# Kernel optimization log

Measured on AMD Instinct MI355X. Metric: run time of the kernel, lower is better.

Reference implementation:

```python
import jax, jax.numpy as jnp
import numpy as np

B, S, IN, OUT = 4, 2048, 4096, 1024
ROUNDS = 12  # prime_factors(4096) == [2]*12
QMIN, QMAX = -128, 127


def _create_noise(key, shape, lo, hi):
    # Obfuscation noise spanning the data range; exactly corrected in forward.
    return jax.random.uniform(key, shape, jnp.float32, -0.5, 0.5) * (hi - lo)


def setup_inputs() -> dict:
    key = jax.random.key(0)
    ks = jax.random.split(key, 6)
    x = jax.random.normal(ks[0], (B, S, IN), jnp.float32)
    weight = jax.random.normal(ks[1], (OUT, IN), jnp.float32) * 0.02
    bias = jax.random.normal(ks[2], (OUT,), jnp.float32) * 0.02
    weight_noise = _create_noise(ks[3], (OUT, IN), weight.min(), weight.max())
    noise_x = _create_noise(ks[4], (B, S, IN), x.min(), x.max())
    # one random permutation of in_features per round
    perms = jnp.stack([jax.random.permutation(jax.random.fold_in(key, 1000 + r), IN)
                       for r in range(ROUNDS)]).astype(jnp.int32)
    # 2048 random orthogonal 2x2 blocks per round (rotations, like ortho_group with dim=2)
    theta = jax.random.uniform(ks[5], (ROUNDS, IN // 2), jnp.float32, 0.0, 2.0 * np.pi)
    c, s = jnp.cos(theta), jnp.sin(theta)
    row0 = jnp.stack([c, -s], axis=-1)
    row1 = jnp.stack([s, c], axis=-1)
    matrices = jnp.stack([row0, row1], axis=-2)  # (ROUNDS, IN//2, 2, 2)
    return {"x": x, "weight": weight, "bias": bias, "weight_noise": weight_noise,
            "noise_x": noise_x, "permutations": perms, "matrices": matrices}


def _permute_matrix_operation(X, perms, mats):
    # X: (..., n, cols). Each round: gather rows by permutation, then apply a
    # block-diagonal orthogonal transform (G blocks of size f along the n axis).
    lead = X.shape[:-2]
    n, cols = X.shape[-2], X.shape[-1]
    G, f = mats.shape[1], mats.shape[2]
    for r in range(mats.shape[0]):
        X = jnp.take(X, perms[r], axis=-2)
        Xb = X.reshape(lead + (G, f, cols))
        X = jnp.einsum('gij,...gjc->...gic', mats[r], Xb).reshape(lead + (n, cols))
    return X


def _quant_dequant(t):
    # Asymmetric per-tensor quantize -> round -> clamp -> dequantize (int8-style).
    lo, hi = t.min(), t.max()
    scale = (hi - lo) / (QMAX - QMIN)
    zp = jnp.round(QMIN - lo / scale)
    q = jnp.clip(jnp.round(t / scale + zp), QMIN, QMAX)
    return (q - zp) * scale


def reference(x, weight, bias, weight_noise, noise_x, permutations, matrices):
    # inverse-transpose blocks; equals `matrices` for orthogonal blocks, kept explicit for fidelity
    inv_mats_mT = jnp.swapaxes(jnp.linalg.inv(matrices), -1, -2)
    w_plus = weight + weight_noise                                   # (OUT, IN)
    permuted_w = jnp.swapaxes(
        _permute_matrix_operation(jnp.swapaxes(w_plus, -1, -2), permutations, inv_mats_mT), -1, -2)
    qw = _quant_dequant(permuted_w)                                  # (OUT, IN)
    permuted_x = jnp.swapaxes(
        _permute_matrix_operation(jnp.swapaxes(x + noise_x, -1, -2), permutations, matrices), -1, -2)
    qx = _quant_dequant(permuted_x)                                  # (B, S, IN)
    res = qx @ qw.T + bias                                           # quantized matmul + bias
    res = res - x @ weight_noise.T                                   # correction term 1
    res = res - noise_x @ w_plus.T                                   # correction term 2
    return res
```

## Files before the change

### kernel.cpp

```cpp
#include <hip/hip_runtime.h>


#define IN_F   4096
#define OUT_F  1024
#define MROWS  8192
#define KTOT   12288
#define KHALF  6144
#define NPASS  6
#define NTIL   96

typedef _Float16 f16;
typedef _Float16 f16x8 __attribute__((ext_vector_type(8)));
typedef _Float16 f16x4 __attribute__((ext_vector_type(4)));
typedef float    f32x4 __attribute__((ext_vector_type(4)));

#define OFF_XT  (0ull)
#define OFF_WT  (OFF_XT + (size_t)MROWS * IN_F * 4)
#define OFF_A   (OFF_WT + (size_t)OUT_F * IN_F * 4)
#define OFF_B   (OFF_A + (size_t)MROWS * KTOT * 2)
#define OFF_MM  (OFF_B + (size_t)OUT_F * KTOT * 2)
#define OFF_TIX (OFF_MM + 256)
#define OFF_TCX (OFF_TIX + (size_t)NPASS * 2048 * 8)
#define OFF_TIW (OFF_TCX + (size_t)NPASS * 2048 * 32)
#define OFF_TCW (OFF_TIW + (size_t)NPASS * 2048 * 8)

#define SW(s) ((s) ^ (((s) >> 3) & 7))

__device__ __forceinline__ unsigned enc_f(float f) {
  unsigned u = __float_as_uint(f);
  return (u & 0x80000000u) ? ~u : (u | 0x80000000u);
}
__device__ __forceinline__ float dec_f(unsigned u) {
  unsigned b = (u & 0x80000000u) ? (u & 0x7fffffffu) : ~u;
  return __uint_as_float(b);
}

__device__ __forceinline__ float4 f4comb(float4 c, float4 x0, float4 x1,
                                         float4 x2, float4 x3) {
  return make_float4(c.x * x0.x + c.y * x1.x + c.z * x2.x + c.w * x3.x,
                     c.x * x0.y + c.y * x1.y + c.z * x2.y + c.w * x3.y,
                     c.x * x0.z + c.y * x1.z + c.z * x2.z + c.w * x3.z,
                     c.x * x0.w + c.y * x1.w + c.z * x2.w + c.w * x3.w);
}

__global__ void build_tables_kernel(const int* __restrict__ perms,
                                    const float* __restrict__ mats,
                                    uint2* __restrict__ tIx, float4* __restrict__ tCx,
                                    uint2* __restrict__ tIw, float4* __restrict__ tCw,
                                    unsigned* __restrict__ mm) {
  if (blockIdx.x == 0 && threadIdx.x == 0) {
    mm[0] = 0xFFFFFFFFu; mm[1] = 0u; mm[2] = 0xFFFFFFFFu; mm[3] = 0u;
  }
  int p = blockIdx.x;
  int r0 = 2 * p, r1 = 2 * p + 1;
  for (int g = threadIdx.x; g < 2048; g += blockDim.x) {
    int q0 = perms[r1 * IN_F + 2 * g], q1 = perms[r1 * IN_F + 2 * g + 1];
    int a0 = q0 >> 1, e0 = q0 & 1, a1 = q1 >> 1, e1 = q1 & 1;
    unsigned i0 = perms[r0 * IN_F + 2 * a0], i1 = perms[r0 * IN_F + 2 * a0 + 1];
    unsigned i2 = perms[r0 * IN_F + 2 * a1], i3 = perms[r0 * IN_F + 2 * a1 + 1];
    uint2 idx = make_uint2(i0 | (i1 << 16), i2 | (i3 << 16));
    const float* Ma = mats + ((size_t)r0 * 2048 + a0) * 4;
    const float* Mb = mats + ((size_t)r0 * 2048 + a1) * 4;
    const float* M1 = mats + ((size_t)r1 * 2048 + g) * 4;
    int o = p * 2048 + g;
    {
      float c00 = Ma[e0 * 2], c01 = Ma[e0 * 2 + 1];
      float c10 = Mb[e1 * 2], c11 = Mb[e1 * 2 + 1];
      float m00 = M1[0], m01 = M1[1], m10 = M1[2], m11 = M1[3];
      tIx[o] = idx;
      tCx[2 * o]     = make_float4(m00 * c00, m00 * c01, m01 * c10, m01 * c11);
      tCx[2 * o + 1] = make_float4(m10 * c00, m10 * c01, m11 * c10, m11 * c11);
    }
    {
      float rda = 1.0f / (Ma[0] * Ma[3] - Ma[1] * Ma[2]);
      float rdb = 1.0f / (Mb[0] * Mb[3] - Mb[1] * Mb[2]);
      float rd1 = 1.0f / (M1[0] * M1[3] - M1[1] * M1[2]);
      float c00 = (e0 == 0 ? Ma[3] : -Ma[1]) * rda;
      float c01 = (e0 == 0 ? -Ma[2] : Ma[0]) * rda;
      float c10 = (e1 == 0 ? Mb[3] : -Mb[1]) * rdb;
      float c11 = (e1 == 0 ? -Mb[2] : Mb[0]) * rdb;
      float m00 = M1[3] * rd1, m01 = -M1[2] * rd1;
      float m10 = -M1[1] * rd1, m11 = M1[0] * rd1;
      tIw[o] = idx;
      tCw[2 * o]     = make_float4(m00 * c00, m00 * c01, m01 * c10, m01 * c11);
      tCw[2 * o + 1] = make_float4(m10 * c00, m10 * c01, m11 * c10, m11 * c11);
    }
  }
}

__global__ __launch_bounds__(1024) void transform_kernel(
    const float* __restrict__ x, const float* __restrict__ nx,
    const float* __restrict__ w, const float* __restrict__ wn,
    const uint2* __restrict__ tIx, const float4* __restrict__ tCx,
    const uint2* __restrict__ tIw, const float4* __restrict__ tCw,
    float* __restrict__ xt, float* __restrict__ wt,
    f16* __restrict__ Aall, f16* __restrict__ Ball,
    unsigned* __restrict__ mm) {
  extern __shared__ float4 buf[];
  const int t = threadIdx.x;
  const bool isW = blockIdx.x >= (MROWS / 4);
  const float *in0, *in1; const uint2* tI; const float4* tC;
  float* tout; f16* fout; int mmidx; size_t m0;
  if (!isW) {
    m0 = (size_t)blockIdx.x * 4;
    in0 = x; in1 = nx; tI = tIx; tC = tCx; tout = xt; fout = Aall; mmidx = 0;
  } else {
    m0 = (size_t)(blockIdx.x - MROWS / 4) * 4;
    in0 = w; in1 = wn; tI = tIw; tC = tCw; tout = wt; fout = Ball; mmidx = 2;
  }

  {
    float4 a0 = ((const float4*)(in0 + (m0 + 0) * IN_F))[t];
    float4 a1 = ((const float4*)(in0 + (m0 + 1) * IN_F))[t];
    float4 a2 = ((const float4*)(in0 + (m0 + 2) * IN_F))[t];
    float4 a3 = ((const float4*)(in0 + (m0 + 3) * IN_F))[t];
    float4 b0 = ((const float4*)(in1 + (m0 + 0) * IN_F))[t];
    float4 b1 = ((const float4*)(in1 + (m0 + 1) * IN_F))[t];
    float4 b2 = ((const float4*)(in1 + (m0 + 2) * IN_F))[t];
    float4 b3 = ((const float4*)(in1 + (m0 + 3) * IN_F))[t];
    float4 s0 = make_float4(a0.x + b0.x, a0.y + b0.y, a0.z + b0.z, a0.w + b0.w);
    float4 s1 = make_float4(a1.x + b1.x, a1.y + b1.y, a1.z + b1.z, a1.w + b1.w);
    float4 s2 = make_float4(a2.x + b2.x, a2.y + b2.y, a2.z + b2.z, a2.w + b2.w);
    float4 s3 = make_float4(a3.x + b3.x, a3.y + b3.y, a3.z + b3.z, a3.w + b3.w);
    int c = t * 4;
    buf[SW(c + 0)] = make_float4(s0.x, s1.x, s2.x, s3.x);
    buf[SW(c + 1)] = make_float4(s0.y, s1.y, s2.y, s3.y);
    buf[SW(c + 2)] = make_float4(s0.z, s1.z, s2.z, s3.z);
    buf[SW(c + 3)] = make_float4(s0.w, s1.w, s2.w, s3.w);
#pragma unroll
    for (int r = 0; r < 4; r++) {
      float4 av = r == 0 ? a0 : r == 1 ? a1 : r == 2 ? a2 : a3;
      float4 bv = r == 0 ? b0 : r == 1 ? b1 : r == 2 ? b2 : b3;
      float4 sv = r == 0 ? s0 : r == 1 ? s1 : r == 2 ? s2 : s3;
      f16* fr = fout + (m0 + r) * KTOT;
      f16x4 p, q;
      if (isW) {
        p.x=(f16)bv.x; p.y=(f16)bv.y; p.z=(f16)bv.z; p.w=(f16)bv.w;
        q.x=(f16)sv.x; q.y=(f16)sv.y; q.z=(f16)sv.z; q.w=(f16)sv.w;
      } else {
        p.x=(f16)(-av.x); p.y=(f16)(-av.y); p.z=(f16)(-av.z); p.w=(f16)(-av.w);
        q.x=(f16)(-bv.x); q.y=(f16)(-bv.y); q.z=(f16)(-bv.z); q.w=(f16)(-bv.w);
      }
      *(f16x4*)(fr + IN_F + c)     = p;
      *(f16x4*)(fr + 2 * IN_F + c) = q;
    }
  }
  __syncthreads();

  int cur = 0;
  for (int pass = 0; pass < NPASS; pass++) {
    const uint2* ti = tI + pass * 2048;
    const float4* tc = tC + (size_t)pass * 4096;
    const float4* bc = buf + cur * 4096;
    float4* bn = buf + (cur ^ 1) * 4096;
#pragma unroll
    for (int i = 0; i < 2; i++) {
      int g = i * 1024 + t;
      uint2 pk = ti[g];
      float4 cA = tc[2 * g], cB = tc[2 * g + 1];
      float4 x0 = bc[SW(pk.x & 0xffff)], x1 = bc[SW(pk.x >> 16)];
      float4 x2 = bc[SW(pk.y & 0xffff)], x3 = bc[SW(pk.y >> 16)];
      bn[SW(2 * g)]     = f4comb(cA, x0, x1, x2, x3);
      bn[SW(2 * g + 1)] = f4comb(cB, x0, x1, x2, x3);
    }
    cur ^= 1;
    __syncthreads();
  }
  float lmin = 3.4e38f, lmax = -3.4e38f;
  {
    int c = t * 4;
    float4 q0 = buf[SW(c + 0)];
    float4 q1 = buf[SW(c + 1)];
    float4 q2 = buf[SW(c + 2)];
    float4 q3 = buf[SW(c + 3)];
    ((float4*)(tout + (m0 + 0) * IN_F))[t] = make_float4(q0.x, q1.x, q2.x, q3.x);
    ((float4*)(tout + (m0 + 1) * IN_F))[t] = make_float4(q0.y, q1.y, q2.y, q3.y);
    ((float4*)(tout + (m0 + 2) * IN_F))[t] = make_float4(q0.z, q1.z, q2.z, q3.z);
    ((float4*)(tout + (m0 + 3) * IN_F))[t] = make_float4(q0.w, q1.w, q2.w, q3.w);
    float mn0 = fminf(fminf(q0.x, q0.y), fminf(q0.z, q0.w));
    float mn1 = fminf(fminf(q1.x, q1.y), fminf(q1.z, q1.w));
    float mn2 = fminf(fminf(q2.x, q2.y), fminf(q2.z, q2.w));
    float mn3 = fminf(fminf(q3.x, q3.y), fminf(q3.z, q3.w));
    float mx0 = fmaxf(fmaxf(q0.x, q0.y), fmaxf(q0.z, q0.w));
    float mx1 = fmaxf(fmaxf(q1.x, q1.y), fmaxf(q1.z, q1.w));
    float mx2 = fmaxf(fmaxf(q2.x, q2.y), fmaxf(q2.z, q2.w));
    float mx3 = fmaxf(fmaxf(q3.x, q3.y), fmaxf(q3.z, q3.w));
    lmin = fminf(fminf(mn0, mn1), fminf(mn2, mn3));
    lmax = fmaxf(fmaxf(mx0, mx1), fmaxf(mx2, mx3));
  }
#pragma unroll
  for (int off = 32; off > 0; off >>= 1) {
    lmin = fminf(lmin, __shfl_down(lmin, off));
    lmax = fmaxf(lmax, __shfl_down(lmax, off));
  }
  float* red = (float*)(buf + 4096);
  int wid = t >> 6;
  if ((t & 63) == 0) { red[wid * 2] = lmin; red[wid * 2 + 1] = lmax; }
  __syncthreads();
  if (t == 0) {
    float bmin = red[0], bmax = red[1];
#pragma unroll
    for (int i = 1; i < 16; i++) {
      bmin = fminf(bmin, red[i * 2]);
      bmax = fmaxf(bmax, red[i * 2 + 1]);
    }
    atomicMin(&mm[mmidx], enc_f(bmin));
    atomicMax(&mm[mmidx + 1], enc_f(bmax));
  }
}

__global__ void finalize_kernel(unsigned* mm) {
  float* sc = (float*)(mm + 4);
  float xlo = dec_f(mm[0]), xhi = dec_f(mm[1]);
  float wlo = dec_f(mm[2]), whi = dec_f(mm[3]);
  float sx = (xhi - xlo) / 255.0f;
  float zx = rintf(-128.0f - xlo / sx);
  float sw = (whi - wlo) / 255.0f;
  float zw = rintf(-128.0f - wlo / sw);
  sc[0] = sx; sc[1] = zx; sc[2] = sw; sc[3] = zw;
}

__global__ __launch_bounds__(256) void quant_kernel(
    const float* __restrict__ xt, const float* __restrict__ wt,
    f16* __restrict__ Aall, f16* __restrict__ Ball,
    const unsigned* __restrict__ mm) {
  const float* sc = (const float*)(mm + 4);
  const bool isW = blockIdx.x >= (MROWS / 4);
  size_t m0 = (size_t)(isW ? blockIdx.x - MROWS / 4 : blockIdx.x) * 4;
  float s = isW ? sc[2] : sc[0], zp = isW ? sc[3] : sc[1];
  int t = threadIdx.x;
#pragma unroll
  for (int r = 0; r < 4; r++) {
    const float4* srow = (const float4*)((isW ? wt : xt) + (m0 + r) * IN_F);
    f16* drow = (isW ? Ball : Aall) + (m0 + r) * KTOT;
#pragma unroll
    for (int j = 0; j < 4; j++) {
      int i4 = j * 256 + t;
      float4 v = srow[i4];
      float q0 = (fminf(fmaxf(rintf(v.x / s + zp), -128.f), 127.f) - zp) * s;
      float q1 = (fminf(fmaxf(rintf(v.y / s + zp), -128.f), 127.f) - zp) * s;
      float q2 = (fminf(fmaxf(rintf(v.z / s + zp), -128.f), 127.f) - zp) * s;
      float q3 = (fminf(fmaxf(rintf(v.w / s + zp), -128.f), 127.f) - zp) * s;
      f16x4 o; o.x = (f16)q0; o.y = (f16)q1; o.z = (f16)q2; o.w = (f16)q3;
      *(f16x4*)(drow + i4 * 4) = o;
    }
  }
}

__global__ __launch_bounds__(256) void bias_init_kernel(
    const float* __restrict__ bias, float* __restrict__ out) {
  const float4* b4 = (const float4*)bias;
  float4* o4 = (float4*)out;
  int idx = blockIdx.x * 256 + threadIdx.x;
  const int total = MROWS * OUT_F / 4;
  for (int i = idx; i < total; i += gridDim.x * 256)
    o4[i] = b4[i & (OUT_F / 4 - 1)];
}

__device__ __forceinline__ void gl2lds16(const void* g, void* l) {
  __builtin_amdgcn_global_load_lds(
      (__attribute__((address_space(1))) void*)g,
      (__attribute__((address_space(3))) void*)l, 16, 0, 0);
}

#define GBAR() asm volatile("s_barrier" ::: "memory")
#define MFMA16(d, va, vb) d = __builtin_amdgcn_mfma_f32_16x16x32_f16(va, vb, d, 0, 0, 0)

#define STAGE(t, hh) do {                                                   \
    const int c_ = (t) & 1;                                                 \
    if ((hh) < 2) {                                                         \
      const f16* g_ = gA + (size_t)((hh) * 128) * KTOT + (size_t)(t) * 64;  \
      f16* l_ = As + c_ * 16384 + (hh) * 8192 + sbase;                      \
      gl2lds16(g_, l_);                                                     \
      gl2lds16(g_ + (size_t)64 * KTOT, l_ + 4096);                          \
    } else {                                                                \
      const f16* g_ = gB + (size_t)(((hh) - 2) * 128) * KTOT + (size_t)(t) * 64; \
      f16* l_ = Bs + c_ * 16384 + ((hh) - 2) * 8192 + sbase;                \
      gl2lds16(g_, l_);                                                     \
      gl2lds16(g_ + (size_t)64 * KTOT, l_ + 4096);                          \
    }                                                                       \
  } while (0)

__global__ __launch_bounds__(512, 2) void gemm_kernel(
    const f16* __restrict__ A, const f16* __restrict__ B,
    float* __restrict__ out) {
  extern __shared__ f16 sm[];
  f16* As = sm;
  f16* Bs = sm + 32768;

  const int tid = threadIdx.x;
  const int wave = tid >> 6, lane = tid & 63;
  const int fr = lane & 15, quad = lane >> 4;
  const int wm = wave >> 2, wn = wave & 3;

  const int orig = blockIdx.x;
  const int wg = (orig & 7) * 32 + (orig >> 3);
  const int ks = wg >> 7;
  const int rem = wg & 127;
  const int bn = rem >> 5, bm = rem & 31;
  const size_t k0 = (size_t)ks * KHALF;

  const int srow = (wave << 3) + (lane >> 3);
  const int scol = (((lane & 7) ^ (lane >> 3)) << 3);
  const f16* gA = A + ((size_t)bm * 256 + srow) * KTOT + k0 + scol;
  const f16* gB = B + ((size_t)bn * 256 + srow) * KTOT + k0 + scol;
  const int sbase = wave << 9;

  const int co0 = ((quad ^ (fr & 7)) << 3);
  const int co1 = co0 ^ 32;
  const f16* rA0 = As + wm * 8192 + fr * 64 + co0;
  const f16* rA1 = As + wm * 8192 + fr * 64 + co1;
  const f16* rB0 = Bs + (wn >> 1) * 8192 + (wn & 1) * 4096 + fr * 64 + co0;
  const f16* rB1 = Bs + (wn >> 1) * 8192 + (wn & 1) * 4096 + fr * 64 + co1;

  f16x8 a0[4][2], a1[4][2], bF[4][2];
  f32x4 acc[8][4] = {};

  STAGE(0, 0); STAGE(0, 1); STAGE(0, 2); STAGE(0, 3);
  STAGE(1, 0); STAGE(1, 1);
  asm volatile("s_waitcnt vmcnt(4)" ::: "memory");
  GBAR();

  for (int t = 0; t < NTIL; ++t) {
    const int c = t & 1;
    const f16* pa0 = rA0 + c * 16384;
    const f16* pa1 = rA1 + c * 16384;
    const f16* pb0 = rB0 + c * 16384;
    const f16* pb1 = rB1 + c * 16384;

#pragma unroll
    for (int i = 0; i < 4; i++) {
      a0[i][0] = *(const f16x8*)(pa0 + i * 1024);
      a0[i][1] = *(const f16x8*)(pa1 + i * 1024);
    }
#pragma unroll
    for (int j = 0; j < 2; j++) {
      bF[j][0] = *(const f16x8*)(pb0 + j * 1024);
      bF[j][1] = *(const f16x8*)(pb1 + j * 1024);
    }
#pragma unroll
    for (int j = 0; j < 2; j++) {
      bF[2 + j][0] = *(const f16x8*)(pb0 + (2 + j) * 1024);
      bF[2 + j][1] = *(const f16x8*)(pb1 + (2 + j) * 1024);
    }
#pragma unroll
    for (int i = 0; i < 4; i++) {
      a1[i][0] = *(const f16x8*)(pa0 + (4 + i) * 1024);
      a1[i][1] = *(const f16x8*)(pa1 + (4 + i) * 1024);
    }
    if (t + 1 < NTIL) STAGE(t + 1, 2);
    GBAR();
    __builtin_amdgcn_s_setprio(1);
#pragma unroll
    for (int i = 0; i < 4; i++)
#pragma unroll
      for (int j = 0; j < 2; j++) {
        MFMA16(acc[i][j], a0[i][0], bF[j][0]);
        MFMA16(acc[i][j], a0[i][1], bF[j][1]);
      }
    __builtin_amdgcn_s_setprio(0);
    GBAR();

    if (t + 1 < NTIL) STAGE(t + 1, 3);
    GBAR();
    __builtin_amdgcn_s_setprio(1);
#pragma unroll
    for (int i = 0; i < 4; i++)
#pragma unroll
      for (int j = 0; j < 2; j++) {
        MFMA16(acc[i][2 + j], a0[i][0], bF[2 + j][0]);
        MFMA16(acc[i][2 + j], a0[i][1], bF[2 + j][1]);
      }
    __builtin_amdgcn_s_setprio(0);
    GBAR();

    if (t + 2 < NTIL) STAGE(t + 2, 0);
    GBAR();
    __builtin_amdgcn_s_setprio(1);
#pragma unroll
    for (int i = 0; i < 4; i++)
#pragma unroll
      for (int j = 0; j < 2; j++) {
        MFMA16(acc[4 + i][j], a1[i][0], bF[j][0]);
        MFMA16(acc[4 + i][j], a1[i][1], bF[j][1]);
      }
    __builtin_amdgcn_s_setprio(0);
    GBAR();

    if (t + 2 < NTIL) STAGE(t + 2, 1);
    GBAR();
    __builtin_amdgcn_s_setprio(1);
#pragma unroll
    for (int i = 0; i < 4; i++)
#pragma unroll
      for (int j = 0; j < 2; j++) {
        MFMA16(acc[4 + i][2 + j], a1[i][0], bF[2 + j][0]);
        MFMA16(acc[4 + i][2 + j], a1[i][1], bF[2 + j][1]);
      }
    __builtin_amdgcn_s_setprio(0);
    if (t + 2 < NTIL) {
      asm volatile("s_waitcnt vmcnt(4)" ::: "memory");
    } else if (t + 1 < NTIL) {
      asm volatile("s_waitcnt vmcnt(0)" ::: "memory");
    }
    GBAR();
  }

  const size_t orow = (size_t)bm * 256 + wm * 128 + quad * 4;
  const int ocol = bn * 256 + wn * 64 + fr;
#pragma unroll
  for (int mi = 0; mi < 8; mi++)
#pragma unroll
    for (int ni = 0; ni < 4; ni++)
#pragma unroll
      for (int e = 0; e < 4; e++)
        unsafeAtomicAdd(&out[(orow + mi * 16 + e) * OUT_F + (ocol + ni * 16)],
                        acc[mi][ni][e]);
}

extern "C" void kernel_launch(void* const* d_in, const int* in_sizes, int n_in,
                              void* d_out, int out_size, void* d_ws, size_t ws_size,
                              hipStream_t stream) {
  const float* x     = (const float*)d_in[0];
  const float* w     = (const float*)d_in[1];
  const float* bias  = (const float*)d_in[2];
  const float* wn    = (const float*)d_in[3];
  const float* nx    = (const float*)d_in[4];
  const int*   perms = (const int*)d_in[5];
  const float* mats  = (const float*)d_in[6];
  float* out = (float*)d_out;

  char* ws = (char*)d_ws;
  float* xt   = (float*)(ws + OFF_XT);
  float* wt   = (float*)(ws + OFF_WT);
  f16*   Aall = (f16*)(ws + OFF_A);
  f16*   Ball = (f16*)(ws + OFF_B);
  unsigned* mm = (unsigned*)(ws + OFF_MM);
  uint2*  tIx = (uint2*)(ws + OFF_TIX);
  float4* tCx = (float4*)(ws + OFF_TCX);
  uint2*  tIw = (uint2*)(ws + OFF_TIW);
  float4* tCw = (float4*)(ws + OFF_TCW);

  static int attr_set = 0;
  if (!attr_set) {
    (void)hipFuncSetAttribute(reinterpret_cast<const void*>(gemm_kernel),
                              hipFuncAttributeMaxDynamicSharedMemorySize, 131072);
    (void)hipFuncSetAttribute(reinterpret_cast<const void*>(transform_kernel),
                              hipFuncAttributeMaxDynamicSharedMemorySize, 131072);
    attr_set = 1;
  }

  build_tables_kernel<<<NPASS, 256, 0, stream>>>(perms, mats, tIx, tCx, tIw, tCw, mm);
  transform_kernel<<<MROWS / 4 + OUT_F / 4, 1024, 131072, stream>>>(
      x, nx, w, wn, tIx, tCx, tIw, tCw, xt, wt, Aall, Ball, mm);
  finalize_kernel<<<1, 1, 0, stream>>>(mm);
  quant_kernel<<<(MROWS + OUT_F) / 4, 256, 0, stream>>>(xt, wt, Aall, Ball, mm);
  bias_init_kernel<<<1024, 256, 0, stream>>>(bias, out);
  gemm_kernel<<<2 * (MROWS / 256) * (OUT_F / 256), 512, 131072, stream>>>(Aall, Ball, out);
}
```

Measured before the change: 684.1 us.

## Merge GEMM barrier phases, fuse bias init into quant, widen table build grid

The GEMM main loop drops from four barrier-separated MFMA phases per tile to two. Each phase now issues two global-to-LDS stages, and an lgkmcnt wait is added before the middle barrier, which cuts synchronisation overhead. The bias-initialisation kernel is folded into the quant kernel as extra blocks, removing one launch. The table-building kernel now uses 48 blocks with one element per thread instead of 6 looping blocks. Fewer barriers may reduce the overlap between loads and MFMAs and change the LDS race margins.

```diff
diff --git a/kernel.cpp b/kernel.cpp
--- a/kernel.cpp
+++ b/kernel.cpp
@@ -43,17 +43,18 @@
                      c.x * x0.w + c.y * x1.w + c.z * x2.w + c.w * x3.w);
 }
 
-__global__ void build_tables_kernel(const int* __restrict__ perms,
-                                    const float* __restrict__ mats,
-                                    uint2* __restrict__ tIx, float4* __restrict__ tCx,
-                                    uint2* __restrict__ tIw, float4* __restrict__ tCw,
-                                    unsigned* __restrict__ mm) {
+__global__ __launch_bounds__(256) void build_tables_kernel(
+    const int* __restrict__ perms, const float* __restrict__ mats,
+    uint2* __restrict__ tIx, float4* __restrict__ tCx,
+    uint2* __restrict__ tIw, float4* __restrict__ tCw,
+    unsigned* __restrict__ mm) {
   if (blockIdx.x == 0 && threadIdx.x == 0) {
     mm[0] = 0xFFFFFFFFu; mm[1] = 0u; mm[2] = 0xFFFFFFFFu; mm[3] = 0u;
   }
-  int p = blockIdx.x;
+  int p = blockIdx.x >> 3;
+  int g = ((blockIdx.x & 7) << 8) + threadIdx.x;
   int r0 = 2 * p, r1 = 2 * p + 1;
-  for (int g = threadIdx.x; g < 2048; g += blockDim.x) {
+  {
     int q0 = perms[r1 * IN_F + 2 * g], q1 = perms[r1 * IN_F + 2 * g + 1];
     int a0 = q0 >> 1, e0 = q0 & 1, a1 = q1 >> 1, e1 = q1 & 1;
     unsigned i0 = perms[r0 * IN_F + 2 * a0], i1 = perms[r0 * IN_F + 2 * a0 + 1];
@@ -220,10 +221,21 @@
   sc[0] = sx; sc[1] = zx; sc[2] = sw; sc[3] = zw;
 }
 
+#define NQB ((MROWS + OUT_F) / 4)
 __global__ __launch_bounds__(256) void quant_kernel(
     const float* __restrict__ xt, const float* __restrict__ wt,
     f16* __restrict__ Aall, f16* __restrict__ Ball,
-    const unsigned* __restrict__ mm) {
+    const unsigned* __restrict__ mm,
+    const float* __restrict__ bias, float* __restrict__ out) {
+  if (blockIdx.x >= NQB) {
+    const float4* b4 = (const float4*)bias;
+    float4* o4 = (float4*)out;
+    int idx = (blockIdx.x - NQB) * 256 + threadIdx.x;
+    const int total = MROWS * OUT_F / 4;
+    for (int i = idx; i < total; i += 512 * 256)
+      o4[i] = b4[i & (OUT_F / 4 - 1)];
+    return;
+  }
   const float* sc = (const float*)(mm + 4);
   const bool isW = blockIdx.x >= (MROWS / 4);
   size_t m0 = (size_t)(isW ? blockIdx.x - MROWS / 4 : blockIdx.x) * 4;
@@ -245,16 +257,6 @@
       *(f16x4*)(drow + i4 * 4) = o;
     }
   }
-}
-
-__global__ __launch_bounds__(256) void bias_init_kernel(
-    const float* __restrict__ bias, float* __restrict__ out) {
-  const float4* b4 = (const float4*)bias;
-  float4* o4 = (float4*)out;
-  int idx = blockIdx.x * 256 + threadIdx.x;
-  const int total = MROWS * OUT_F / 4;
-  for (int i = idx; i < total; i += gridDim.x * 256)
-    o4[i] = b4[i & (OUT_F / 4 - 1)];
 }
 
 __device__ __forceinline__ void gl2lds16(const void* g, void* l) {
@@ -334,70 +336,41 @@
       a0[i][1] = *(const f16x8*)(pa1 + i * 1024);
     }
 #pragma unroll
-    for (int j = 0; j < 2; j++) {
+    for (int j = 0; j < 4; j++) {
       bF[j][0] = *(const f16x8*)(pb0 + j * 1024);
       bF[j][1] = *(const f16x8*)(pb1 + j * 1024);
-    }
-#pragma unroll
-    for (int j = 0; j < 2; j++) {
-      bF[2 + j][0] = *(const f16x8*)(pb0 + (2 + j) * 1024);
-      bF[2 + j][1] = *(const f16x8*)(pb1 + (2 + j) * 1024);
     }
 #pragma unroll
     for (int i = 0; i < 4; i++) {
       a1[i][0] = *(const f16x8*)(pa0 + (4 + i) * 1024);
       a1[i][1] = *(const f16x8*)(pa1 + (4 + i) * 1024);
     }
-    if (t + 1 < NTIL) STAGE(t + 1, 2);
-    GBAR();
+    if (t + 1 < NTIL) { STAGE(t + 1, 2); STAGE(t + 1, 3); }
+
     __builtin_amdgcn_s_setprio(1);
 #pragma unroll
     for (int i = 0; i < 4; i++)
 #pragma unroll
-      for (int j = 0; j < 2; j++) {
+      for (int j = 0; j < 4; j++) {
         MFMA16(acc[i][j], a0[i][0], bF[j][0]);
         MFMA16(acc[i][j], a0[i][1], bF[j][1]);
       }
     __builtin_amdgcn_s_setprio(0);
+
+    asm volatile("s_waitcnt lgkmcnt(0)" ::: "memory");
     GBAR();
-
-    if (t + 1 < NTIL) STAGE(t + 1, 3);
-    GBAR();
+    if (t + 2 < NTIL) { STAGE(t + 2, 0); STAGE(t + 2, 1); }
+
     __builtin_amdgcn_s_setprio(1);
 #pragma unroll
     for (int i = 0; i < 4; i++)
 #pragma unroll
-      for (int j = 0; j < 2; j++) {
-        MFMA16(acc[i][2 + j], a0[i][0], bF[2 + j][0]);
-        MFMA16(acc[i][2 + j], a0[i][1], bF[2 + j][1]);
-      }
-    __builtin_amdgcn_s_setprio(0);
-    GBAR();
-
-    if (t + 2 < NTIL) STAGE(t + 2, 0);
-    GBAR();
-    __builtin_amdgcn_s_setprio(1);
-#pragma unroll
-    for (int i = 0; i < 4; i++)
-#pragma unroll
-      for (int j = 0; j < 2; j++) {
+      for (int j = 0; j < 4; j++) {
         MFMA16(acc[4 + i][j], a1[i][0], bF[j][0]);
         MFMA16(acc[4 + i][j], a1[i][1], bF[j][1]);
       }
     __builtin_amdgcn_s_setprio(0);
-    GBAR();
-
-    if (t + 2 < NTIL) STAGE(t + 2, 1);
-    GBAR();
-    __builtin_amdgcn_s_setprio(1);
-#pragma unroll
-    for (int i = 0; i < 4; i++)
-#pragma unroll
-      for (int j = 0; j < 2; j++) {
-        MFMA16(acc[4 + i][2 + j], a1[i][0], bF[2 + j][0]);
-        MFMA16(acc[4 + i][2 + j], a1[i][1], bF[2 + j][1]);
-      }
-    __builtin_amdgcn_s_setprio(0);
+
     if (t + 2 < NTIL) {
       asm volatile("s_waitcnt vmcnt(4)" ::: "memory");
     } else if (t + 1 < NTIL) {
@@ -450,11 +423,10 @@
     attr_set = 1;
   }
 
-  build_tables_kernel<<<NPASS, 256, 0, stream>>>(perms, mats, tIx, tCx, tIw, tCw, mm);
+  build_tables_kernel<<<48, 256, 0, stream>>>(perms, mats, tIx, tCx, tIw, tCw, mm);
   transform_kernel<<<MROWS / 4 + OUT_F / 4, 1024, 131072, stream>>>(
       x, nx, w, wn, tIx, tCx, tIw, tCw, xt, wt, Aall, Ball, mm);
   finalize_kernel<<<1, 1, 0, stream>>>(mm);
-  quant_kernel<<<(MROWS + OUT_F) / 4, 256, 0, stream>>>(xt, wt, Aall, Ball, mm);
-  bias_init_kernel<<<1024, 256, 0, stream>>>(bias, out);
+  quant_kernel<<<NQB + 512, 256, 0, stream>>>(xt, wt, Aall, Ball, mm, bias, out);
   gemm_kernel<<<2 * (MROWS / 256) * (OUT_F / 256), 512, 131072, stream>>>(Aall, Ball, out);
 }
```

New measurement: 661.5 us. 1.03x faster.
